# Performance work log

Hardware: AMD Instinct MI355X
Metric: run time of the kernel (lower is better)

The kernel has to match this reference:

```python
import jax, jax.numpy as jnp
import numpy as np

N = 65536        # number of encoding vectors (flattened tokens)
K = 1024         # num_embeddings (codebook size)
D = 128          # embedding_dim
BETA = 0.25


def setup_inputs() -> dict:
    key = jax.random.key(0)
    k_enc, k_cb = jax.random.split(key)
    encoding = jax.random.normal(k_enc, (N, D), dtype=jnp.float32)
    # nn.Embedding weight initialized uniform(-1/K, 1/K)
    codebook = jax.random.uniform(k_cb, (K, D), dtype=jnp.float32,
                                  minval=-1.0 / K, maxval=1.0 / K)
    return {"encoding": encoding, "codebook": codebook}


def reference(encoding, codebook):
    # Nearest codebook entry per row. argmin of L2 distance == argmin of
    # squared distance; expand ||e - w||^2 = ||e||^2 - 2 e.w + ||w||^2.
    # ||e||^2 is constant per row, so it does not affect the argmin.
    scores = (-2.0 * jnp.einsum('nd,kd->nk', encoding, codebook)
              + jnp.sum(codebook * codebook, axis=-1)[None, :])  # [N, K]
    quantized_index = jnp.argmin(scores, axis=-1)                # [N] int
    quantized_embedding = codebook[quantized_index]              # [N, D] gather == onehot @ W

    sg = jax.lax.stop_gradient
    commitment_loss = jnp.mean((sg(quantized_embedding) - encoding) ** 2)
    embedding_loss = jnp.mean((quantized_embedding - sg(encoding)) ** 2)
    vq_loss = commitment_loss * BETA + embedding_loss

    # straight-through estimator
    quantized_st = encoding + sg(quantized_embedding - encoding)

    quantized_index = quantized_index[:, None]  # match torch unsqueeze(1) -> [N, 1]
    return (quantized_index, quantized_st, vq_loss, embedding_loss, commitment_loss)
```

## Files before the change

### kernel.cpp

```cpp
#include <hip/hip_runtime.h>


#define NROWS 65536
#define KCB   1024
#define DIM   128
#define DV    32
#define MSE_DENOM 8388608.0f
#define MARGIN 3.0e-5f
#define FLAGCAP 16384
#define CSCALE   1024.0f
#define CDESCALE 0.0009765625f

#define WS_CNORM_F 256
#define WS_LIST_B  8192
#define WS_PH_B    73728
#define WS_NEEDED  335872

typedef __attribute__((ext_vector_type(16))) float float16v;
typedef _Float16 half8 __attribute__((ext_vector_type(8)));
union U4H8 { uint4 u; half8 h; };
union F4A  { float4 v; float f[4]; };
union HU   { _Float16 f; unsigned short u; };

__device__ __forceinline__ unsigned umn(unsigned a, unsigned b) { return a < b ? a : b; }
__device__ __forceinline__ unsigned umx(unsigned a, unsigned b) { return a > b ? a : b; }
__device__ __forceinline__ float unmap_score(unsigned up) {
  return (up & 0x80000000u) ? __uint_as_float(up ^ 0x80000000u) : __uint_as_float(~up);
}
__device__ __forceinline__ void gload16(const void* g, void* s) {
  __builtin_amdgcn_global_load_lds((const __attribute__((address_space(1))) unsigned int*)g,
                                   (__attribute__((address_space(3))) unsigned int*)s,
                                   16, 0, 0);
}

__global__ __launch_bounds__(64) void vq_prep0(const float* __restrict__ C,
                                               float* __restrict__ wsf) {
  int k = blockIdx.x * 64 + threadIdx.x;
  if (k == 0) { wsf[0] = 0.0f; ((unsigned*)wsf)[1] = 0u; }
  const float4* c4 = (const float4*)C + (size_t)k * DV;
  float s = 0.f;
#pragma unroll 8
  for (int i = 0; i < DV; ++i) {
    float4 v = c4[i];
    s = fmaf(v.x, v.x, s); s = fmaf(v.y, v.y, s);
    s = fmaf(v.z, v.z, s); s = fmaf(v.w, v.w, s);
  }
  wsf[WS_CNORM_F + k] = s;
}

__global__ __launch_bounds__(256) void vq_pack(const float* __restrict__ C,
                                               uint4* __restrict__ PH) {
  int g = blockIdx.x * 256 + threadIdx.x;
  int mt = g >> 9, s = (g >> 6) & 7, l = g & 63;
  int cw = mt * 32 + (l & 31);
  int k0 = s * 16 + (l >> 5) * 8;
  const float* src = C + (size_t)cw * DIM + k0;
  float4 x0 = *(const float4*)src;
  float4 x1 = *(const float4*)(src + 4);
  unsigned h[8];
  {
    float v[8] = {x0.x, x0.y, x0.z, x0.w, x1.x, x1.y, x1.z, x1.w};
#pragma unroll
    for (int j = 0; j < 8; ++j) { HU u; u.f = (_Float16)(CSCALE * v[j]); h[j] = u.u; }
  }
  PH[g] = make_uint4(h[0] | (h[1] << 16), h[2] | (h[3] << 16),
                     h[4] | (h[5] << 16), h[6] | (h[7] << 16));
}

__global__ __launch_bounds__(128, 2) void vq_main6(const float* __restrict__ E,
                                                   const float* __restrict__ C,
                                                   float* __restrict__ wsf,
                                                   float* __restrict__ out) {
  __shared__ uint4 SH[2][1024];
  __shared__ __align__(16) float CN[1024];
  __shared__ int BI[64];

  const int tid  = threadIdx.x;
  const int w    = tid >> 6;
  const int l    = tid & 63;
  const int half = l >> 5;
  const int rr   = l & 31;
  const int row0 = blockIdx.x * 64;

  const uint4* PHg = (const uint4*)((const char*)wsf + WS_PH_B);

  {
    const uint4* sh = PHg + tid;
#pragma unroll
    for (int k = 0; k < 8; ++k)
      gload16(sh + k * 128, &SH[0][0] + tid + k * 128);
    const uint4* cn = ((const uint4*)(wsf + WS_CNORM_F)) + tid;
    gload16(cn,       ((uint4*)CN) + tid);
    gload16(cn + 128, ((uint4*)CN) + tid + 128);
  }

  half8 beh[8];
  float s2 = 0.f;
  const float* erow = E + (size_t)(row0 + w * 32 + rr) * DIM + half * 8;
#pragma unroll
  for (int s = 0; s < 8; ++s) {
    float4 x0 = *(const float4*)(erow + s * 16);
    float4 x1 = *(const float4*)(erow + s * 16 + 4);
    float v[8] = {x0.x, x0.y, x0.z, x0.w, x1.x, x1.y, x1.z, x1.w};
#pragma unroll
    for (int j = 0; j < 8; ++j) {
      float y = v[j];
      s2 = fmaf(y, y, s2);
      beh[s][j] = (_Float16)(-2.f * y);
    }
  }

  asm volatile("s_waitcnt vmcnt(0)" ::: "memory");
  __syncthreads();

  unsigned best = 0xFFFFFFFFu, second = 0xFFFFFFFFu;

  for (int t = 0; t < 16; ++t) {
    const int b = t & 1;
    if (t < 15) {
      const uint4* sh = PHg + (size_t)(t + 1) * 1024 + tid;
      uint4* dh = &SH[b ^ 1][0];
#pragma unroll
      for (int k = 0; k < 8; ++k)
        gload16(sh + k * 128, dh + tid + k * 128);
    }

    float16v a0 = {0,0,0,0,0,0,0,0,0,0,0,0,0,0,0,0};
    float16v a1 = {0,0,0,0,0,0,0,0,0,0,0,0,0,0,0,0};
    float16v b0 = {0,0,0,0,0,0,0,0,0,0,0,0,0,0,0,0};
    float16v b1 = {0,0,0,0,0,0,0,0,0,0,0,0,0,0,0,0};
#pragma unroll
    for (int s = 0; s < 8; s += 2) {
      U4H8 hA0, hA1, hB0, hB1;
      hA0.u = SH[b][s * 64 + l];
      hA1.u = SH[b][(s + 1) * 64 + l];
      hB0.u = SH[b][512 + s * 64 + l];
      hB1.u = SH[b][512 + (s + 1) * 64 + l];
      a0 = __builtin_amdgcn_mfma_f32_32x32x16_f16(hA0.h, beh[s],     a0, 0, 0, 0);
      a1 = __builtin_amdgcn_mfma_f32_32x32x16_f16(hA1.h, beh[s + 1], a1, 0, 0, 0);
      b0 = __builtin_amdgcn_mfma_f32_32x32x16_f16(hB0.h, beh[s],     b0, 0, 0, 0);
      b1 = __builtin_amdgcn_mfma_f32_32x32x16_f16(hB1.h, beh[s + 1], b1, 0, 0, 0);
    }

#pragma unroll
    for (int tt = 0; tt < 2; ++tt) {
      const int tg = t * 2 + tt;
      const unsigned cwb = (unsigned)(tg * 32 + half * 4);
#pragma unroll
      for (int q = 0; q < 4; ++q) {
        F4A a; a.v = *(const float4*)&CN[tg * 32 + q * 8 + half * 4];
#pragma unroll
        for (int i = 0; i < 4; ++i) {
          float acc = tt ? (b0[q * 4 + i] + b1[q * 4 + i])
                         : (a0[q * 4 + i] + a1[q * 4 + i]);
          float sc = fmaf(acc, CDESCALE, a.f[i]);
          unsigned u = __float_as_uint(sc);
          u ^= ((unsigned)(((int)u) >> 31)) | 0x80000000u;
          u = (u & 0xFFFFFC00u) | (cwb + (unsigned)(q * 8 + i));
          unsigned nb = umn(best, u);
          second = umn(second, umx(best, u));
          best = nb;
        }
      }
    }

    asm volatile("s_waitcnt vmcnt(0)" ::: "memory");
    __syncthreads();
  }

  unsigned ob = (unsigned)__shfl_xor((int)best, 32, 64);
  unsigned os = (unsigned)__shfl_xor((int)second, 32, 64);
  unsigned ns = umn(umn(second, os), umx(best, ob));
  unsigned nb = umn(best, ob);
  float en = s2 + __shfl_xor(s2, 32, 64);

  if (half == 0) {
    const int r = w * 32 + rr;
    int   bi = (int)(nb & 1023u);
    float bv = unmap_score(nb & 0xFFFFFC00u);
    float sv = unmap_score(ns & 0xFFFFFC00u);
    out[row0 + r] = (float)bi;
    BI[r] = bi;
    if (sv - bv < MARGIN) {
      unsigned idx = atomicAdd((unsigned*)wsf + 1, 1u);
      if (idx < FLAGCAP) ((int*)((char*)wsf + WS_LIST_B))[idx] = row0 + r;
    }
    float term = en + bv;
#pragma unroll
    for (int off = 16; off > 0; off >>= 1) term += __shfl_down(term, off);
    if (rr == 0) atomicAdd(wsf, term);
  }
  __syncthreads();

  const float4* C4   = (const float4*)C;
  float4*       out4 = (float4*)out;
#pragma unroll
  for (int it = 0; it < 16; ++it) {
    int flat = it * 128 + tid;
    int r = flat >> 5, d4 = flat & 31;
    out4[(NROWS / 4) + (size_t)(row0 + r) * DV + d4] = C4[(size_t)BI[r] * DV + d4];
  }
}

__global__ __launch_bounds__(256) void vq_fix(const float* __restrict__ E,
                                              const float* __restrict__ C,
                                              float* __restrict__ wsf,
                                              float* __restrict__ out) {
  __shared__ float4 eL[4][32];
  __shared__ float  RV[4][4];
  __shared__ int    RI[4][4];
  __shared__ int    RESi[4];
  const int tid = threadIdx.x;
  const int wv  = tid >> 6;
  const int ln  = tid & 63;
  const int* list = (const int*)((const char*)wsf + WS_LIST_B);
  int nf = (int)((const unsigned*)wsf)[1];
  if (nf > FLAGCAP) nf = FLAGCAP;
  const float4* E4 = (const float4*)E;
  const float4* C4 = (const float4*)C;
  const float*  cn = wsf + WS_CNORM_F;
  float4* out4 = (float4*)out;

  for (int g = blockIdx.x; g * 4 < nf; g += gridDim.x) {
    const int base = g * 4;
    if (tid < 128) {
      int r = tid >> 5, d4 = tid & 31;
      int R = (base + r < nf) ? list[base + r] : list[base];
      eL[r][d4] = E4[(size_t)R * DV + d4];
    }
    __syncthreads();
    float bv[4] = {3.0e38f, 3.0e38f, 3.0e38f, 3.0e38f};
    int   bi[4] = {0, 0, 0, 0};
#pragma unroll
    for (int j = 0; j < 4; ++j) {
      int k = j * 256 + tid;
      float d0 = 0.f, d1 = 0.f, d2 = 0.f, d3 = 0.f;
#pragma unroll 4
      for (int d4 = 0; d4 < 32; ++d4) {
        float4 c = C4[(size_t)k * DV + d4];
        float4 e0 = eL[0][d4], e1 = eL[1][d4], e2 = eL[2][d4], e3 = eL[3][d4];
        d0 = fmaf(c.x, e0.x, d0); d0 = fmaf(c.y, e0.y, d0);
        d0 = fmaf(c.z, e0.z, d0); d0 = fmaf(c.w, e0.w, d0);
        d1 = fmaf(c.x, e1.x, d1); d1 = fmaf(c.y, e1.y, d1);
        d1 = fmaf(c.z, e1.z, d1); d1 = fmaf(c.w, e1.w, d1);
        d2 = fmaf(c.x, e2.x, d2); d2 = fmaf(c.y, e2.y, d2);
        d2 = fmaf(c.z, e2.z, d2); d2 = fmaf(c.w, e2.w, d2);
        d3 = fmaf(c.x, e3.x, d3); d3 = fmaf(c.y, e3.y, d3);
        d3 = fmaf(c.z, e3.z, d3); d3 = fmaf(c.w, e3.w, d3);
      }
      float cnk = cn[k];
      float s0 = fmaf(-2.f, d0, cnk);
      float s1 = fmaf(-2.f, d1, cnk);
      float s2 = fmaf(-2.f, d2, cnk);
      float s3 = fmaf(-2.f, d3, cnk);
      if (s0 < bv[0] || (s0 == bv[0] && k < bi[0])) { bv[0] = s0; bi[0] = k; }
      if (s1 < bv[1] || (s1 == bv[1] && k < bi[1])) { bv[1] = s1; bi[1] = k; }
      if (s2 < bv[2] || (s2 == bv[2] && k < bi[2])) { bv[2] = s2; bi[2] = k; }
      if (s3 < bv[3] || (s3 == bv[3] && k < bi[3])) { bv[3] = s3; bi[3] = k; }
    }
#pragma unroll
    for (int off = 32; off > 0; off >>= 1) {
#pragma unroll
      for (int r = 0; r < 4; ++r) {
        float wv_ = __shfl_down(bv[r], off);
        int   ji  = __shfl_down(bi[r], off);
        if (wv_ < bv[r] || (wv_ == bv[r] && ji < bi[r])) { bv[r] = wv_; bi[r] = ji; }
      }
    }
    if (ln == 0) {
#pragma unroll
      for (int r = 0; r < 4; ++r) { RV[wv][r] = bv[r]; RI[wv][r] = bi[r]; }
    }
    __syncthreads();
    if (tid < 4) {
      float v = RV[0][tid]; int i = RI[0][tid];
#pragma unroll
      for (int q = 1; q < 4; ++q) {
        float vv = RV[q][tid]; int ii = RI[q][tid];
        if (vv < v || (vv == v && ii < i)) { v = vv; i = ii; }
      }
      RESi[tid] = i;
      if (base + tid < nf) out[list[base + tid]] = (float)i;
    }
    __syncthreads();
    if (tid < 128) {
      int r = tid >> 5, d4 = tid & 31;
      if (base + r < nf) {
        int R = list[base + r];
        out4[(NROWS / 4) + (size_t)R * DV + d4] = C4[(size_t)RESi[r] * DV + d4];
      }
    }
    __syncthreads();
  }
}

__global__ void vq_final(const float* __restrict__ wsf, float* __restrict__ out) {
  if (threadIdx.x == 0 && blockIdx.x == 0) {
    float mse = wsf[0] / MSE_DENOM;
    out[NROWS + NROWS * DIM + 0] = 1.25f * mse;
    out[NROWS + NROWS * DIM + 1] = mse;
    out[NROWS + NROWS * DIM + 2] = mse;
  }
}

__global__ __launch_bounds__(256) void vq_prep_fb(const float* __restrict__ C,
                                                  float* __restrict__ ws) {
  int k = blockIdx.x * 256 + threadIdx.x;
  if (k == 0) ws[0] = 0.0f;
  const float4* c4 = (const float4*)C + (size_t)k * DV;
  float s = 0.f;
#pragma unroll 8
  for (int i = 0; i < DV; ++i) {
    float4 v = c4[i];
    s = fmaf(v.x, v.x, s); s = fmaf(v.y, v.y, s);
    s = fmaf(v.z, v.z, s); s = fmaf(v.w, v.w, s);
  }
  ws[64 + k] = s;
}

__global__ __launch_bounds__(256) void vq_main_fb(const float* __restrict__ E,
                                                  const float* __restrict__ C,
                                                  const float* __restrict__ cnorm,
                                                  float* __restrict__ out,
                                                  float* __restrict__ lossacc) {
  __shared__ float smem[16384];
  float4* EsV = (float4*)smem;
  float4* CsV = (float4*)(smem + 8192);
  const int tid  = threadIdx.x;
  const int row0 = blockIdx.x * 64;
#pragma unroll
  for (int i = 0; i < 8; ++i) {
    int flat = i * 256 + tid;
    int r = flat >> 5, d4 = flat & 31;
    EsV[r * 32 + (d4 ^ (r & 31))] = ((const float4*)E)[(size_t)(row0 + r) * DV + d4];
  }
  const int tx = tid & 15, ty = tid >> 4;
  int rbase[4], rmask[4];
#pragma unroll
  for (int i = 0; i < 4; ++i) { int r = i * 16 + ty; rbase[i] = r * 32; rmask[i] = r & 31; }
  float bestv[4]; int besti[4];
#pragma unroll
  for (int i = 0; i < 4; ++i) { bestv[i] = 3.0e38f; besti[i] = 0; }
  for (int ch = 0; ch < 16; ++ch) {
    const int k0 = ch * 64;
    __syncthreads();
#pragma unroll
    for (int i = 0; i < 8; ++i) {
      int flat = i * 256 + tid;
      int k = flat >> 5, d4 = flat & 31;
      CsV[k * 32 + (d4 ^ (k & 31))] = ((const float4*)C)[(size_t)(k0 + k) * DV + d4];
    }
    __syncthreads();
    float acc[4][4] = {};
#pragma unroll 8
    for (int d4 = 0; d4 < DV; ++d4) {
      float4 a[4], b[4];
#pragma unroll
      for (int i = 0; i < 4; ++i) a[i] = EsV[rbase[i] + (d4 ^ rmask[i])];
#pragma unroll
      for (int j = 0; j < 4; ++j) { int k = j * 16 + tx; b[j] = CsV[k * 32 + (d4 ^ (k & 31))]; }
#pragma unroll
      for (int i = 0; i < 4; ++i)
#pragma unroll
        for (int j = 0; j < 4; ++j) {
          acc[i][j] = fmaf(a[i].x, b[j].x, acc[i][j]);
          acc[i][j] = fmaf(a[i].y, b[j].y, acc[i][j]);
          acc[i][j] = fmaf(a[i].z, b[j].z, acc[i][j]);
          acc[i][j] = fmaf(a[i].w, b[j].w, acc[i][j]);
        }
    }
#pragma unroll
    for (int j = 0; j < 4; ++j) {
      int kg = k0 + j * 16 + tx;
      float cnv = cnorm[kg];
#pragma unroll
      for (int i = 0; i < 4; ++i) {
        float s = fmaf(-2.0f, acc[i][j], cnv);
        if (s < bestv[i] || (s == bestv[i] && kg < besti[i])) { bestv[i] = s; besti[i] = kg; }
      }
    }
  }
  float* Rv = smem + 8192;
  int*   Ri = (int*)(smem + 9216);
  int*   BIf = (int*)(smem + 10240);
  __syncthreads();
#pragma unroll
  for (int i = 0; i < 4; ++i) {
    int r = i * 16 + ty;
    Rv[r * 16 + tx] = bestv[i];
    Ri[r * 16 + tx] = besti[i];
  }
  __syncthreads();
  if (tid < 64) {
    const int r = tid;
    float bv = Rv[r * 16]; int bi = Ri[r * 16];
#pragma unroll
    for (int t = 1; t < 16; ++t) {
      float v = Rv[r * 16 + t]; int ii = Ri[r * 16 + t];
      if (v < bv || (v == bv && ii < bi)) { bv = v; bi = ii; }
    }
    float en = 0.f;
#pragma unroll 8
    for (int d4 = 0; d4 < DV; ++d4) {
      float4 v = EsV[r * 32 + (d4 ^ (r & 31))];
      en = fmaf(v.x, v.x, en); en = fmaf(v.y, v.y, en);
      en = fmaf(v.z, v.z, en); en = fmaf(v.w, v.w, en);
    }
    out[row0 + r] = (float)bi;
    BIf[r] = bi;
    float blocksum = en + bv;
#pragma unroll
    for (int off = 32; off > 0; off >>= 1) blocksum += __shfl_down(blocksum, off);
    if (tid == 0) atomicAdd(lossacc, blocksum);
  }
  __syncthreads();
  const float4* C4   = (const float4*)C;
  float4*       out4 = (float4*)out;
  for (int flat = tid; flat < 64 * DV; flat += 256) {
    int r = flat >> 5, d4 = flat & 31;
    out4[(NROWS / 4) + (size_t)(row0 + r) * DV + d4] = C4[(size_t)BIf[r] * DV + d4];
  }
}

__global__ void vq_final_fb(const float* __restrict__ ws, float* __restrict__ out) {
  if (threadIdx.x == 0 && blockIdx.x == 0) {
    float mse = ws[0] / MSE_DENOM;
    out[NROWS + NROWS * DIM + 0] = 1.25f * mse;
    out[NROWS + NROWS * DIM + 1] = mse;
    out[NROWS + NROWS * DIM + 2] = mse;
  }
}

extern "C" void kernel_launch(void* const* d_in, const int* in_sizes, int n_in,
                              void* d_out, int out_size, void* d_ws, size_t ws_size,
                              hipStream_t stream) {
  const float* E = (const float*)d_in[0];
  const float* C = (const float*)d_in[1];
  float* out = (float*)d_out;
  float* wsf = (float*)d_ws;

  if (ws_size >= (size_t)WS_NEEDED) {
    uint4* PH = (uint4*)((char*)d_ws + WS_PH_B);
    vq_prep0<<<16, 64, 0, stream>>>(C, wsf);
    vq_pack<<<64, 256, 0, stream>>>(C, PH);
    vq_main6<<<NROWS / 64, 128, 0, stream>>>(E, C, wsf, out);
    vq_fix<<<256, 256, 0, stream>>>(E, C, wsf, out);
    vq_final<<<1, 64, 0, stream>>>(wsf, out);
  } else {
    vq_prep_fb<<<4, 256, 0, stream>>>(C, wsf);
    vq_main_fb<<<NROWS / 64, 256, 0, stream>>>(E, C, wsf + 64, out, wsf);
    vq_final_fb<<<1, 64, 0, stream>>>(wsf, out);
  }
}
```

Before: 166.8 us.

## Enlarge main kernel to 256 rows per block with register-staged codebook tiles

The main kernel moves from 64 rows per 128-thread block to 256 rows per 512-thread block. Each shared-memory codebook tile is 64KB and is reused by eight waves, and codebook loads are staged through registers instead of global_load_lds. The MFMA accumulator is seeded with prescaled codebook norms, so the norm add is folded into the matrix op. The packed-key umin/umax argmin is replaced by float fmed3/fmin tracking with an explicit index. This cuts codebook traffic per row and the epilogue ALU work, but the larger shared footprint (over 128KB) permits only one block per CU and lowers occupancy.

```diff
diff --git a/kernel.cpp b/kernel.cpp
--- a/kernel.cpp
+++ b/kernel.cpp
@@ -11,26 +11,21 @@
 #define CSCALE   1024.0f
 #define CDESCALE 0.0009765625f
 
-#define WS_CNORM_F 256
-#define WS_LIST_B  8192
-#define WS_PH_B    73728
-#define WS_NEEDED  335872
+#define WS_CNORM_F  256
+#define WS_CN1024_F 1280
+#define WS_LIST_B   12288
+#define WS_PH_B     77824
+#define WS_NEEDED   339968
 
 typedef __attribute__((ext_vector_type(16))) float float16v;
 typedef _Float16 half8 __attribute__((ext_vector_type(8)));
 union U4H8 { uint4 u; half8 h; };
 union F4A  { float4 v; float f[4]; };
+union F16V { float16v v; float f[16]; };
 union HU   { _Float16 f; unsigned short u; };
 
-__device__ __forceinline__ unsigned umn(unsigned a, unsigned b) { return a < b ? a : b; }
-__device__ __forceinline__ unsigned umx(unsigned a, unsigned b) { return a > b ? a : b; }
-__device__ __forceinline__ float unmap_score(unsigned up) {
-  return (up & 0x80000000u) ? __uint_as_float(up ^ 0x80000000u) : __uint_as_float(~up);
-}
-__device__ __forceinline__ void gload16(const void* g, void* s) {
-  __builtin_amdgcn_global_load_lds((const __attribute__((address_space(1))) unsigned int*)g,
-                                   (__attribute__((address_space(3))) unsigned int*)s,
-                                   16, 0, 0);
+__device__ __forceinline__ float fmed3(float a, float b, float c) {
+  return __builtin_amdgcn_fmed3f(a, b, c);
 }
 
 __global__ __launch_bounds__(64) void vq_prep0(const float* __restrict__ C,
@@ -45,7 +40,8 @@
     s = fmaf(v.x, v.x, s); s = fmaf(v.y, v.y, s);
     s = fmaf(v.z, v.z, s); s = fmaf(v.w, v.w, s);
   }
-  wsf[WS_CNORM_F + k] = s;
+  wsf[WS_CNORM_F + k]  = s;
+  wsf[WS_CN1024_F + k] = s * CSCALE;
 }
 
 __global__ __launch_bounds__(256) void vq_pack(const float* __restrict__ C,
@@ -67,32 +63,29 @@
                      h[4] | (h[5] << 16), h[6] | (h[7] << 16));
 }
 
-__global__ __launch_bounds__(128, 2) void vq_main6(const float* __restrict__ E,
+__global__ __launch_bounds__(512, 1) void vq_main7(const float* __restrict__ E,
                                                    const float* __restrict__ C,
                                                    float* __restrict__ wsf,
                                                    float* __restrict__ out) {
-  __shared__ uint4 SH[2][1024];
+  __shared__ uint4 SB[2][4096];
   __shared__ __align__(16) float CN[1024];
-  __shared__ int BI[64];
+  __shared__ int BI[256];
 
   const int tid  = threadIdx.x;
   const int w    = tid >> 6;
   const int l    = tid & 63;
   const int half = l >> 5;
   const int rr   = l & 31;
-  const int row0 = blockIdx.x * 64;
+  const int row0 = blockIdx.x * 256;
 
   const uint4* PHg = (const uint4*)((const char*)wsf + WS_PH_B);
-
-  {
-    const uint4* sh = PHg + tid;
-#pragma unroll
-    for (int k = 0; k < 8; ++k)
-      gload16(sh + k * 128, &SH[0][0] + tid + k * 128);
-    const uint4* cn = ((const uint4*)(wsf + WS_CNORM_F)) + tid;
-    gload16(cn,       ((uint4*)CN) + tid);
-    gload16(cn + 128, ((uint4*)CN) + tid + 128);
-  }
+  const uint4* CNg = (const uint4*)(wsf + WS_CN1024_F);
+
+  uint4 stg[8];
+#pragma unroll
+  for (int j = 0; j < 8; ++j) stg[j] = PHg[j * 512 + tid];
+  uint4 cnr;
+  if (tid < 256) cnr = CNg[tid];
 
   half8 beh[8];
   float s2 = 0.f;
@@ -110,77 +103,69 @@
     }
   }
 
-  asm volatile("s_waitcnt vmcnt(0)" ::: "memory");
+#pragma unroll
+  for (int j = 0; j < 8; ++j) SB[0][j * 512 + tid] = stg[j];
+  if (tid < 256) ((uint4*)CN)[tid] = cnr;
   __syncthreads();
 
-  unsigned best = 0xFFFFFFFFu, second = 0xFFFFFFFFu;
-
-  for (int t = 0; t < 16; ++t) {
-    const int b = t & 1;
-    if (t < 15) {
-      const uint4* sh = PHg + (size_t)(t + 1) * 1024 + tid;
-      uint4* dh = &SH[b ^ 1][0];
-#pragma unroll
-      for (int k = 0; k < 8; ++k)
-        gload16(sh + k * 128, dh + tid + k * 128);
-    }
-
-    float16v a0 = {0,0,0,0,0,0,0,0,0,0,0,0,0,0,0,0};
-    float16v a1 = {0,0,0,0,0,0,0,0,0,0,0,0,0,0,0,0};
-    float16v b0 = {0,0,0,0,0,0,0,0,0,0,0,0,0,0,0,0};
-    float16v b1 = {0,0,0,0,0,0,0,0,0,0,0,0,0,0,0,0};
-#pragma unroll
-    for (int s = 0; s < 8; s += 2) {
-      U4H8 hA0, hA1, hB0, hB1;
-      hA0.u = SH[b][s * 64 + l];
-      hA1.u = SH[b][(s + 1) * 64 + l];
-      hB0.u = SH[b][512 + s * 64 + l];
-      hB1.u = SH[b][512 + (s + 1) * 64 + l];
-      a0 = __builtin_amdgcn_mfma_f32_32x32x16_f16(hA0.h, beh[s],     a0, 0, 0, 0);
-      a1 = __builtin_amdgcn_mfma_f32_32x32x16_f16(hA1.h, beh[s + 1], a1, 0, 0, 0);
-      b0 = __builtin_amdgcn_mfma_f32_32x32x16_f16(hB0.h, beh[s],     b0, 0, 0, 0);
-      b1 = __builtin_amdgcn_mfma_f32_32x32x16_f16(hB1.h, beh[s + 1], b1, 0, 0, 0);
-    }
-
-#pragma unroll
-    for (int tt = 0; tt < 2; ++tt) {
-      const int tg = t * 2 + tt;
-      const unsigned cwb = (unsigned)(tg * 32 + half * 4);
+  float m1 = 3.0e38f, m2 = 3.0e38f;
+  int bi0 = 0;
+
+  for (int qt = 0; qt < 4; ++qt) {
+    const int b = qt & 1;
+    if (qt < 3) {
+#pragma unroll
+      for (int j = 0; j < 8; ++j) stg[j] = PHg[(qt + 1) * 4096 + j * 512 + tid];
+    }
+    const int kq = qt * 256;
+
+#pragma unroll
+    for (int tt = 0; tt < 8; ++tt) {
+      const int tg = qt * 8 + tt;
+      U4H8 h[8];
+#pragma unroll
+      for (int s = 0; s < 8; ++s) h[s].u = SB[b][tt * 512 + s * 64 + l];
+      F16V acc;
 #pragma unroll
       for (int q = 0; q < 4; ++q) {
-        F4A a; a.v = *(const float4*)&CN[tg * 32 + q * 8 + half * 4];
-#pragma unroll
-        for (int i = 0; i < 4; ++i) {
-          float acc = tt ? (b0[q * 4 + i] + b1[q * 4 + i])
-                         : (a0[q * 4 + i] + a1[q * 4 + i]);
-          float sc = fmaf(acc, CDESCALE, a.f[i]);
-          unsigned u = __float_as_uint(sc);
-          u ^= ((unsigned)(((int)u) >> 31)) | 0x80000000u;
-          u = (u & 0xFFFFFC00u) | (cwb + (unsigned)(q * 8 + i));
-          unsigned nb = umn(best, u);
-          second = umn(second, umx(best, u));
-          best = nb;
-        }
-      }
-    }
-
-    asm volatile("s_waitcnt vmcnt(0)" ::: "memory");
-    __syncthreads();
-  }
-
-  unsigned ob = (unsigned)__shfl_xor((int)best, 32, 64);
-  unsigned os = (unsigned)__shfl_xor((int)second, 32, 64);
-  unsigned ns = umn(umn(second, os), umx(best, ob));
-  unsigned nb = umn(best, ob);
-  float en = s2 + __shfl_xor(s2, 32, 64);
+        F4A c; c.v = *(const float4*)&CN[tg * 32 + q * 8 + half * 4];
+        acc.f[q * 4 + 0] = c.f[0]; acc.f[q * 4 + 1] = c.f[1];
+        acc.f[q * 4 + 2] = c.f[2]; acc.f[q * 4 + 3] = c.f[3];
+      }
+#pragma unroll
+      for (int s = 0; s < 8; ++s)
+        acc.v = __builtin_amdgcn_mfma_f32_32x32x16_f16(h[s].h, beh[s], acc.v, 0, 0, 0);
+#pragma unroll
+      for (int reg = 0; reg < 16; ++reg) {
+        float sc = acc.f[reg] * CDESCALE;
+        m2 = fmed3(sc, m1, m2);
+        if (sc < m1) bi0 = kq + tt * 32 + (reg >> 2) * 8 + (reg & 3);
+        m1 = fminf(m1, sc);
+      }
+    }
+
+    if (qt < 3) {
+#pragma unroll
+      for (int j = 0; j < 8; ++j) SB[b ^ 1][j * 512 + tid] = stg[j];
+    }
+    __syncthreads();
+  }
+
+  int   bi  = bi0 + half * 4;
+  float obm  = __shfl_xor(m1, 32, 64);
+  float obm2 = __shfl_xor(m2, 32, 64);
+  int   obi  = __shfl_xor(bi, 32, 64);
+  float oen  = __shfl_xor(s2, 32, 64);
+  float sv = fminf(fminf(m2, obm2), fmaxf(m1, obm));
+  float bv; int bif;
+  if (obm < m1 || (obm == m1 && obi < bi)) { bv = obm; bif = obi; }
+  else                                     { bv = m1;  bif = bi;  }
+  float en = s2 + oen;
 
   if (half == 0) {
     const int r = w * 32 + rr;
-    int   bi = (int)(nb & 1023u);
-    float bv = unmap_score(nb & 0xFFFFFC00u);
-    float sv = unmap_score(ns & 0xFFFFFC00u);
-    out[row0 + r] = (float)bi;
-    BI[r] = bi;
+    out[row0 + r] = (float)bif;
+    BI[r] = bif;
     if (sv - bv < MARGIN) {
       unsigned idx = atomicAdd((unsigned*)wsf + 1, 1u);
       if (idx < FLAGCAP) ((int*)((char*)wsf + WS_LIST_B))[idx] = row0 + r;
@@ -196,7 +181,7 @@
   float4*       out4 = (float4*)out;
 #pragma unroll
   for (int it = 0; it < 16; ++it) {
-    int flat = it * 128 + tid;
+    int flat = it * 512 + tid;
     int r = flat >> 5, d4 = flat & 31;
     out4[(NROWS / 4) + (size_t)(row0 + r) * DV + d4] = C4[(size_t)BI[r] * DV + d4];
   }
@@ -443,7 +428,7 @@
     uint4* PH = (uint4*)((char*)d_ws + WS_PH_B);
     vq_prep0<<<16, 64, 0, stream>>>(C, wsf);
     vq_pack<<<64, 256, 0, stream>>>(C, PH);
-    vq_main6<<<NROWS / 64, 128, 0, stream>>>(E, C, wsf, out);
+    vq_main7<<<NROWS / 256, 512, 0, stream>>>(E, C, wsf, out);
     vq_fix<<<256, 256, 0, stream>>>(E, C, wsf, out);
     vq_final<<<1, 64, 0, stream>>>(wsf, out);
   } else {
```

New measurement: 178.6 us. 7.1% more time.
